# Kernel tuning notes

Hardware: AMD Instinct MI355X
Metric: run time of the kernel (lower is better)

Reference implementation:

```python
import jax, jax.numpy as jnp
import numpy as np

L, D, H, DK, FF, R, N, B = 8, 256, 8, 32, 1024, 37, 1024, 1
EPS = 1e-6


def setup_inputs() -> dict:
    key = jax.random.key(0)
    ks = jax.random.split(key, 16)
    def w(i, shape, s=0.05):
        return jax.random.normal(ks[i], shape, jnp.float32) * s
    return {
        "x": jax.random.normal(ks[0], (B, N, D), jnp.float32),
        "relations": jax.random.randint(ks[1], (N, N), 0, R),
        "Wq": w(2, (L, D, D)), "bq": jnp.zeros((L, D), jnp.float32),
        "Wk": w(3, (L, D, D)), "bk": jnp.zeros((L, D), jnp.float32),
        "Wv": w(4, (L, D, D)), "bv": jnp.zeros((L, D), jnp.float32),
        "Wo": w(5, (L, D, D)), "bo": jnp.zeros((L, D), jnp.float32),
        "rel_k_emb": w(6, (L, R, DK)), "rel_v_emb": w(7, (L, R, DK)),
        "W1": w(8, (L, D, FF)), "b1": jnp.zeros((L, FF), jnp.float32),
        "W2": w(9, (L, FF, D)), "b2": jnp.zeros((L, D), jnp.float32),
        "ln1_g": jnp.ones((L, D), jnp.float32), "ln1_b": jnp.zeros((L, D), jnp.float32),
        "ln2_g": jnp.ones((L, D), jnp.float32), "ln2_b": jnp.zeros((L, D), jnp.float32),
        "lnf_g": jnp.ones((D,), jnp.float32), "lnf_b": jnp.zeros((D,), jnp.float32),
    }


def _layernorm(h, g, b):
    # Annotated-Transformer LayerNorm: g*(x-mu)/(std+eps)+b with unbiased std
    mu = h.mean(-1, keepdims=True)
    sd = jnp.sqrt(h.var(-1, keepdims=True, ddof=1))
    return g * (h - mu) / (sd + EPS) + b


def reference(x, relations, Wq, bq, Wk, bk, Wv, bv, Wo, bo,
              rel_k_emb, rel_v_emb, W1, b1, W2, b2,
              ln1_g, ln1_b, ln2_g, ln2_b, lnf_g, lnf_b):
    Bb, n, d = x.shape
    scale = 1.0 / jnp.sqrt(jnp.float32(DK))
    for l in range(L):
        # --- relation-aware self-attention sublayer (pre-norm residual) ---
        xn = _layernorm(x, ln1_g[l], ln1_b[l])
        q = (xn @ Wq[l] + bq[l]).reshape(Bb, n, H, DK).transpose(0, 2, 1, 3)
        k = (xn @ Wk[l] + bk[l]).reshape(Bb, n, H, DK).transpose(0, 2, 1, 3)
        v = (xn @ Wv[l] + bv[l]).reshape(Bb, n, H, DK).transpose(0, 2, 1, 3)
        rk = rel_k_emb[l][relations]  # [n, n, DK] irregular gather
        rv = rel_v_emb[l][relations]  # [n, n, DK]
        scores = (jnp.einsum('bhid,bhjd->bhij', q, k)
                  + jnp.einsum('bhid,ijd->bhij', q, rk)) * scale
        p = jax.nn.softmax(scores, axis=-1)
        o = (jnp.einsum('bhij,bhjd->bhid', p, v)
             + jnp.einsum('bhij,ijd->bhid', p, rv))
        o = o.transpose(0, 2, 1, 3).reshape(Bb, n, d) @ Wo[l] + bo[l]
        x = x + o
        # --- position-wise FFN sublayer (pre-norm residual) ---
        xn = _layernorm(x, ln2_g[l], ln2_b[l])
        x = x + (jax.nn.relu(xn @ W1[l] + b1[l]) @ W2[l] + b2[l])
    return _layernorm(x, lnf_g, lnf_b)
```

## Files before the change

kernel.cpp:

```cpp
#include <hip/hip_runtime.h>
#include <stdint.h>

#define L_ 8
#define D_ 256
#define H_ 8
#define DK_ 32
#define FF_ 1024
#define R_ 37
#define N_ 1024
#define AIB 16

#define SCL (0.17677669529663689f * 1.4426950408889634f)

typedef float f4v __attribute__((ext_vector_type(4)));
typedef short b8v __attribute__((ext_vector_type(8)));
typedef uint  u2v __attribute__((ext_vector_type(2)));

__device__ __forceinline__ ushort f2b(float f){
  union { float f; uint32_t u; } x; x.f = f;
  return (ushort)((x.u + 0x7FFFu + ((x.u >> 16) & 1u)) >> 16);
}
__device__ __forceinline__ float b2f(ushort u){
  union { uint32_t u; float f; } x; x.u = ((uint32_t)u) << 16;
  return x.f;
}
__device__ __forceinline__ uint pk2b(float lo, float hi){
  return (((uint)f2b(hi)) << 16) | (uint)f2b(lo);
}
__device__ __forceinline__ float ex2(float x){ return __builtin_amdgcn_exp2f(x); }

__device__ __forceinline__ void lds_fadd(float* p, float v){
  asm volatile("ds_add_f32 %0, %1" :: "v"((uint)(uintptr_t)p), "v"(v) : "memory");
}

__global__ __launch_bounds__(256)
void wcast_kernel(const float* __restrict__ src, ushort* __restrict__ dst, int K, int Nc){
  __shared__ float t[32][33];
  int l = blockIdx.z;
  long base = (long)l * K * Nc;
  int n0 = blockIdx.x * 32, k0 = blockIdx.y * 32;
  int tx = threadIdx.x, ty = threadIdx.y;
  #pragma unroll
  for (int r = 0; r < 32; r += 8)
    t[ty + r][tx] = src[base + (long)(k0 + ty + r) * Nc + n0 + tx];
  __syncthreads();
  #pragma unroll
  for (int r = 0; r < 32; r += 8)
    dst[base + (long)(n0 + ty + r) * K + k0 + tx] = f2b(t[tx][ty + r]);
}

__global__ __launch_bounds__(256)
void rel8_kernel(const int* __restrict__ rel, uint* __restrict__ rel8){
  long idx = (long)blockIdx.x * 256 + threadIdx.x;
  int4 v = ((const int4*)rel)[idx];
  rel8[idx] = (uint)(v.x & 255) | ((uint)(v.y & 255) << 8)
            | ((uint)(v.z & 255) << 16) | ((uint)(v.w & 255) << 24);
}

template<int OUTB>
__global__ __launch_bounds__(64)
void ln_kernel(const float* __restrict__ x, const float* __restrict__ g, const float* __restrict__ b,
               ushort* __restrict__ ob, float* __restrict__ of){
  int row = blockIdx.x, lane = threadIdx.x;
  float4 v = ((const float4*)(x + (long)row * D_))[lane];
  float s = v.x + v.y + v.z + v.w;
  float s2 = v.x*v.x + v.y*v.y + v.z*v.z + v.w*v.w;
  #pragma unroll
  for (int o = 32; o; o >>= 1){ s += __shfl_xor(s, o); s2 += __shfl_xor(s2, o); }
  float mu = s * (1.f / D_);
  float var = (s2 - D_ * mu * mu) * (1.f / (D_ - 1));
  var = fmaxf(var, 0.f);
  float inv = 1.f / (sqrtf(var) + 1e-6f);
  float4 gv = ((const float4*)g)[lane];
  float4 bv = ((const float4*)b)[lane];
  float o0 = gv.x * (v.x - mu) * inv + bv.x;
  float o1 = gv.y * (v.y - mu) * inv + bv.y;
  float o2 = gv.z * (v.z - mu) * inv + bv.z;
  float o3 = gv.w * (v.w - mu) * inv + bv.w;
  if (OUTB){
    ushort4 u; u.x = f2b(o0); u.y = f2b(o1); u.z = f2b(o2); u.w = f2b(o3);
    ((ushort4*)ob)[(long)row * 64 + lane] = u;
  } else {
    float4 o; o.x = o0; o.y = o1; o.z = o2; o.w = o3;
    ((float4*)of)[(long)row * 64 + lane] = o;
  }
}

template<int QKV, int RELU, int RESID, int OUTF, int OUTB>
__global__ __launch_bounds__(256)
void gemm_kernel(const ushort* __restrict__ A,
                 const ushort* __restrict__ W0, const ushort* __restrict__ W1p, const ushort* __restrict__ W2p,
                 const float* __restrict__ B0, const float* __restrict__ B1p, const float* __restrict__ B2p,
                 float* __restrict__ resid, float* __restrict__ outF, ushort* __restrict__ outB,
                 ushort* __restrict__ outB2,
                 int M, int Nc, int K){
  __shared__ ushort Al[64 * 48];
  __shared__ ushort Bl[64 * 48];
  int tid = threadIdx.x;
  int lane = tid & 63, w = tid >> 6;
  int wm = w >> 1, wn = w & 1;
  int bn0 = blockIdx.x * 64, bm0 = blockIdx.y * 64;
  const ushort* WT; const float* bias; int wn0;
  if (QKV){
    int which = bn0 >> 8;
    WT = which == 0 ? W0 : (which == 1 ? W1p : W2p);
    bias = which == 0 ? B0 : (which == 1 ? B1p : B2p);
    wn0 = bn0 & 255;
  } else { WT = W0; bias = B0; wn0 = bn0; }

  int r4 = tid >> 2, c8 = (tid & 3) * 8;
  const ushort* ag = A + (long)(bm0 + r4) * K + c8;
  const ushort* bg = WT + (long)(wn0 + r4) * K + c8;

  f4v acc[2][2];
  #pragma unroll
  for (int i = 0; i < 2; ++i)
    #pragma unroll
    for (int j = 0; j < 2; ++j)
      acc[i][j] = (f4v){0.f, 0.f, 0.f, 0.f};

  int l16 = lane & 15, lg = lane >> 4;
  int arow0 = (wm * 32 + l16) * 48 + lg * 8;
  int brow0 = (wn * 32 + l16) * 48 + lg * 8;

  for (int k0 = 0; k0 < K; k0 += 32){
    b8v a8 = *(const b8v*)(ag + k0);
    b8v b8 = *(const b8v*)(bg + k0);
    __syncthreads();
    *(b8v*)&Al[r4 * 48 + c8] = a8;
    *(b8v*)&Bl[r4 * 48 + c8] = b8;
    __syncthreads();
    b8v a0 = *(const b8v*)&Al[arow0];
    b8v a1 = *(const b8v*)&Al[arow0 + 16 * 48];
    b8v b0 = *(const b8v*)&Bl[brow0];
    b8v b1 = *(const b8v*)&Bl[brow0 + 16 * 48];
    acc[0][0] = __builtin_amdgcn_mfma_f32_16x16x32_bf16(a0, b0, acc[0][0], 0, 0, 0);
    acc[0][1] = __builtin_amdgcn_mfma_f32_16x16x32_bf16(a0, b1, acc[0][1], 0, 0, 0);
    acc[1][0] = __builtin_amdgcn_mfma_f32_16x16x32_bf16(a1, b0, acc[1][0], 0, 0, 0);
    acc[1][1] = __builtin_amdgcn_mfma_f32_16x16x32_bf16(a1, b1, acc[1][1], 0, 0, 0);
  }
  #pragma unroll
  for (int fi = 0; fi < 2; ++fi)
    #pragma unroll
    for (int fj = 0; fj < 2; ++fj){
      int row0 = bm0 + wm * 32 + fi * 16 + lg * 4;
      int col = bn0 + wn * 32 + fj * 16 + l16;
      float vv[4];
      #pragma unroll
      for (int j = 0; j < 4; ++j) vv[j] = acc[fi][fj][j] + bias[QKV ? (col & 255) : col];
      if (QKV){
        int which = col >> 8, hh = (col >> 5) & 7, dk = col & 31;
        if (which == 2){
          ushort4 pk; pk.x = f2b(vv[0]); pk.y = f2b(vv[1]); pk.z = f2b(vv[2]); pk.w = f2b(vv[3]);
          *(ushort4*)(outB2 + (long)hh * 32768 + (long)dk * 1024 + row0) = pk;
        } else {
          #pragma unroll
          for (int j = 0; j < 4; ++j)
            outB[(long)which * 262144 + (long)hh * 32768 + (long)(row0 + j) * 32 + dk] = f2b(vv[j]);
        }
      } else {
        #pragma unroll
        for (int j = 0; j < 4; ++j){
          float v = vv[j];
          if (RELU) v = fmaxf(v, 0.f);
          long idx = (long)(row0 + j) * Nc + col;
          if (RESID) v += resid[idx];
          if (OUTF) outF[idx] = v;
          if (OUTB) outB[idx] = f2b(v);
        }
      }
    }
}

__global__ __launch_bounds__(512)
void attn_kernel(const ushort* __restrict__ qb, const ushort* __restrict__ kb,
                 const ushort* __restrict__ vbt, const float* __restrict__ rke,
                 const float* __restrict__ rve,
                 const unsigned char* __restrict__ rel8, ushort* __restrict__ ob){
  __shared__ float q_l[AIB * 32];
  __shared__ float qr_l[AIB * 40];
  __shared__ float prb[8 * AIB * 41];
  __shared__ uint  p_l[8 * AIB * 20];
  __shared__ float part_l[8 * AIB * 33];
  __shared__ float wf_l[8 * AIB];
  __shared__ float ls_l[8 * AIB];
  __shared__ float lrow_l[AIB];

  int tid = threadIdx.x, lane = tid & 63, w = tid >> 6;
  int l16 = lane & 15, g = lane >> 4;
  int ib0 = blockIdx.x * AIB, h = blockIdx.y;
  int ir = l16;

  if (tid < 128){
    int row = tid >> 3, d4 = (tid & 7) * 4;
    ushort4 u = *(const ushort4*)(qb + (long)((h << 10) + ib0 + row) * 32 + d4);
    q_l[row * 32 + d4 + 0] = b2f(u.x);
    q_l[row * 32 + d4 + 1] = b2f(u.y);
    q_l[row * 32 + d4 + 2] = b2f(u.z);
    q_l[row * 32 + d4 + 3] = b2f(u.w);
  }
  for (int idx = tid; idx < 8 * AIB * 41; idx += 512) prb[idx] = 0.f;
  __syncthreads();

  for (int slot = tid; slot < AIB * 40; slot += 512){
    int row = slot / 40, r = slot - row * 40;
    if (r < R_){
      const float* qh = &q_l[row * 32];
      const float* e = rke + r * 32;
      float acc = 0.f;
      #pragma unroll
      for (int d = 0; d < 32; ++d) acc += qh[d] * e[d];
      qr_l[slot] = acc * SCL;
    }
  }
  __syncthreads();

  b8v qf = *(const b8v*)(qb + (long)((h << 10) + ib0 + ir) * 32 + g * 8);

  f4v oacc0 = (f4v){0.f,0.f,0.f,0.f}, oacc1 = (f4v){0.f,0.f,0.f,0.f};
  float m = -3.0e38f;
  const float* qrr = &qr_l[ir * 40];
  float* prr = &prb[(w * AIB + ir) * 41];
  const unsigned char* relrow = rel8 + (long)(ib0 + ir) * N_ + w * 128;
  const ushort* kbh = kb + (long)(h << 10) * 32;
  const ushort* vth = vbt + (long)h * 32 * 1024;
  uint* pw = &p_l[(w * AIB + l16) * 20];

  uint raw[8];
  #pragma unroll
  for (int t = 0; t < 4; ++t){
    raw[t * 2]     = *(const uint*)(relrow + t * 32 + g * 4);
    raw[t * 2 + 1] = *(const uint*)(relrow + t * 32 + 16 + g * 4);
  }
  float qv[32];
  #pragma unroll
  for (int t = 0; t < 4; ++t)
    #pragma unroll
    for (int e = 0; e < 4; ++e){
      qv[t * 8 + e]     = qrr[(raw[t * 2]     >> (8 * e)) & 255];
      qv[t * 8 + 4 + e] = qrr[(raw[t * 2 + 1] >> (8 * e)) & 255];
    }

  int jb = w * 128;
  b8v kf0c = *(const b8v*)(kbh + (long)(jb + l16) * 32 + g * 8);
  b8v kf1c = *(const b8v*)(kbh + (long)(jb + 16 + l16) * 32 + g * 8);
  b8v vt0c = *(const b8v*)(vth + (long)l16 * 1024 + jb + g * 8);
  b8v vt1c = *(const b8v*)(vth + (long)(16 + l16) * 1024 + jb + g * 8);

  #pragma unroll
  for (int t = 0; t < 4; ++t){
    int j1 = jb + ((t + 1) & 3) * 32;
    b8v kf0n = *(const b8v*)(kbh + (long)(j1 + l16) * 32 + g * 8);
    b8v kf1n = *(const b8v*)(kbh + (long)(j1 + 16 + l16) * 32 + g * 8);
    b8v vt0n = *(const b8v*)(vth + (long)l16 * 1024 + j1 + g * 8);
    b8v vt1n = *(const b8v*)(vth + (long)(16 + l16) * 1024 + j1 + g * 8);

    f4v z = (f4v){0.f,0.f,0.f,0.f};
    f4v s0 = __builtin_amdgcn_mfma_f32_16x16x32_bf16(kf0c, qf, z, 0, 0, 0);
    f4v s1 = __builtin_amdgcn_mfma_f32_16x16x32_bf16(kf1c, qf, z, 0, 0, 0);

    float sv[8];
    #pragma unroll
    for (int e = 0; e < 4; ++e){
      sv[e]     = s0[e] * SCL + qv[t * 8 + e];
      sv[e + 4] = s1[e] * SCL + qv[t * 8 + 4 + e];
    }
    float lmax = sv[0];
    #pragma unroll
    for (int e = 1; e < 8; ++e) lmax = fmaxf(lmax, sv[e]);

    if (__any(lmax - m > 12.f)){
      float tmax = fmaxf(lmax, __shfl_xor(lmax, 16));
      tmax = fmaxf(tmax, __shfl_xor(tmax, 32));
      if (tmax > m){
        float f = ex2(m - tmax);
        oacc0 *= f; oacc1 *= f;
        #pragma unroll
        for (int b2 = 0; b2 < 10; ++b2){
          int bi = g * 10 + b2;
          if (bi < R_) prr[bi] *= f;
        }
        m = tmax;
      }
    }
    float p[8];
    #pragma unroll
    for (int e = 0; e < 8; ++e) p[e] = ex2(sv[e] - m);
    #pragma unroll
    for (int e = 0; e < 4; ++e){
      lds_fadd(&prr[(raw[t * 2]     >> (8 * e)) & 255], p[e]);
      lds_fadd(&prr[(raw[t * 2 + 1] >> (8 * e)) & 255], p[e + 4]);
    }

    uint pk0 = pk2b(p[0], p[1]), pk1 = pk2b(p[2], p[3]);
    uint pk2 = pk2b(p[4], p[5]), pk3 = pk2b(p[6], p[7]);
    *(u2v*)&pw[g * 2]     = (u2v){pk0, pk1};
    *(u2v*)&pw[8 + g * 2] = (u2v){pk2, pk3};
    b8v pf = *(const b8v*)&pw[g * 4];
    oacc0 = __builtin_amdgcn_mfma_f32_16x16x32_bf16(vt0c, pf, oacc0, 0, 0, 0);
    oacc1 = __builtin_amdgcn_mfma_f32_16x16x32_bf16(vt1c, pf, oacc1, 0, 0, 0);

    kf0c = kf0n; kf1c = kf1n; vt0c = vt0n; vt1c = vt1n;
  }

  {
    float* pp = &part_l[(w * AIB + ir) * 33];
    #pragma unroll
    for (int e = 0; e < 4; ++e){
      pp[g * 4 + e] = oacc0[e];
      pp[16 + g * 4 + e] = oacc1[e];
    }
    if (g == 0) pp[32] = m;
  }
  __syncthreads();

  for (int slot = tid; slot < 8 * AIB; slot += 512){
    const float* pb = &prb[slot * 41];
    float acc = 0.f;
    #pragma unroll
    for (int r = 0; r < R_; ++r) acc += pb[r];
    ls_l[slot] = acc;
  }
  __syncthreads();

  if (tid < AIB){
    int row = tid;
    float mstar = -3.0e38f;
    #pragma unroll
    for (int s = 0; s < 8; ++s) mstar = fmaxf(mstar, part_l[(s * AIB + row) * 33 + 32]);
    float lstar = 0.f;
    #pragma unroll
    for (int s = 0; s < 8; ++s){
      float wfv = ex2(part_l[(s * AIB + row) * 33 + 32] - mstar);
      wf_l[s * AIB + row] = wfv;
      lstar += ls_l[s * AIB + row] * wfv;
    }
    lrow_l[row] = lstar;
  }
  __syncthreads();

  for (int slot = tid; slot < AIB * 41; slot += 512){
    int row = slot / 41;
    float acc = 0.f;
    #pragma unroll
    for (int s = 0; s < 8; ++s) acc += prb[s * AIB * 41 + slot] * wf_l[s * AIB + row];
    prb[slot] = acc;
  }
  __syncthreads();

  {
    int row = tid >> 5, d = tid & 31;
    float o1 = 0.f;
    #pragma unroll
    for (int s = 0; s < 8; ++s) o1 += part_l[(s * AIB + row) * 33 + d] * wf_l[s * AIB + row];
    float o2 = 0.f;
    #pragma unroll
    for (int r = 0; r < R_; ++r) o2 += prb[row * 41 + r] * rve[r * 32 + d];
    float val = (o1 + o2) / lrow_l[row];
    ob[(long)(ib0 + row) * D_ + h * 32 + d] = f2b(val);
  }
}

extern "C" void kernel_launch(void* const* d_in, const int* in_sizes, int n_in,
                              void* d_out, int out_size, void* d_ws, size_t ws_size,
                              hipStream_t stream){
  const float* x    = (const float*)d_in[0];
  const int*   rel  = (const int*)d_in[1];
  const float* Wq   = (const float*)d_in[2];
  const float* bq   = (const float*)d_in[3];
  const float* Wk   = (const float*)d_in[4];
  const float* bk   = (const float*)d_in[5];
  const float* Wv   = (const float*)d_in[6];
  const float* bv   = (const float*)d_in[7];
  const float* Wo   = (const float*)d_in[8];
  const float* bo   = (const float*)d_in[9];
  const float* rke  = (const float*)d_in[10];
  const float* rve  = (const float*)d_in[11];
  const float* W1   = (const float*)d_in[12];
  const float* b1   = (const float*)d_in[13];
  const float* W2   = (const float*)d_in[14];
  const float* b2   = (const float*)d_in[15];
  const float* ln1g = (const float*)d_in[16];
  const float* ln1b = (const float*)d_in[17];
  const float* ln2g = (const float*)d_in[18];
  const float* ln2b = (const float*)d_in[19];
  const float* lnfg = (const float*)d_in[20];
  const float* lnfb = (const float*)d_in[21];

  char* wsb = (char*)d_ws;
  size_t off = 0;
  auto alloc = [&](size_t bytes){ void* p = wsb + off; off += (bytes + 255) & ~255ull; return p; };
  float*  xw   = (float*) alloc((size_t)N_ * D_ * 4);
  ushort* qkvb = (ushort*)alloc((size_t)3 * H_ * N_ * DK_ * 2);
  ushort* vbt  = (ushort*)alloc((size_t)H_ * DK_ * N_ * 2);
  ushort* xnb  = (ushort*)alloc((size_t)N_ * D_ * 2);
  ushort* obf  = (ushort*)alloc((size_t)N_ * D_ * 2);
  ushort* hidb = (ushort*)alloc((size_t)N_ * FF_ * 2);
  uint*   rel8 = (uint*)  alloc((size_t)N_ * N_);
  ushort* wqT  = (ushort*)alloc((size_t)L_ * D_ * D_ * 2);
  ushort* wkT  = (ushort*)alloc((size_t)L_ * D_ * D_ * 2);
  ushort* wvT  = (ushort*)alloc((size_t)L_ * D_ * D_ * 2);
  ushort* woT  = (ushort*)alloc((size_t)L_ * D_ * D_ * 2);
  ushort* w1T  = (ushort*)alloc((size_t)L_ * D_ * FF_ * 2);
  ushort* w2T  = (ushort*)alloc((size_t)L_ * D_ * FF_ * 2);
  (void)ws_size; (void)in_sizes; (void)n_in; (void)out_size;

  ushort* qb = qkvb;
  ushort* kb = qkvb + (size_t)H_ * N_ * DK_;

  dim3 tb(32, 8);
  wcast_kernel<<<dim3(D_/32,  D_/32,  L_), tb, 0, stream>>>(Wq, wqT, D_, D_);
  wcast_kernel<<<dim3(D_/32,  D_/32,  L_), tb, 0, stream>>>(Wk, wkT, D_, D_);
  wcast_kernel<<<dim3(D_/32,  D_/32,  L_), tb, 0, stream>>>(Wv, wvT, D_, D_);
  wcast_kernel<<<dim3(D_/32,  D_/32,  L_), tb, 0, stream>>>(Wo, woT, D_, D_);
  wcast_kernel<<<dim3(FF_/32, D_/32,  L_), tb, 0, stream>>>(W1, w1T, D_, FF_);
  wcast_kernel<<<dim3(D_/32,  FF_/32, L_), tb, 0, stream>>>(W2, w2T, FF_, D_);
  rel8_kernel<<<N_ * N_ / 1024, 256, 0, stream>>>(rel, rel8);

  hipMemcpyAsync(xw, x, (size_t)N_ * D_ * 4, hipMemcpyDeviceToDevice, stream);

  for (int l = 0; l < L_; ++l){
    ln_kernel<1><<<N_, 64, 0, stream>>>(xw, ln1g + l * D_, ln1b + l * D_, xnb, nullptr);
    gemm_kernel<1,0,0,0,1><<<dim3(768/64, N_/64), 256, 0, stream>>>(
        xnb, wqT + (size_t)l * D_ * D_, wkT + (size_t)l * D_ * D_, wvT + (size_t)l * D_ * D_,
        bq + l * D_, bk + l * D_, bv + l * D_,
        nullptr, nullptr, qkvb, vbt, N_, 768, D_);
    attn_kernel<<<dim3(N_/AIB, H_), 512, 0, stream>>>(
        qb, kb, vbt, rke + (size_t)l * R_ * DK_, rve + (size_t)l * R_ * DK_,
        (const unsigned char*)rel8, obf);
    gemm_kernel<0,0,1,1,0><<<dim3(D_/64, N_/64), 256, 0, stream>>>(
        obf, woT + (size_t)l * D_ * D_, nullptr, nullptr,
        bo + l * D_, nullptr, nullptr,
        xw, xw, nullptr, nullptr, N_, D_, D_);
    ln_kernel<1><<<N_, 64, 0, stream>>>(xw, ln2g + l * D_, ln2b + l * D_, xnb, nullptr);
    gemm_kernel<0,1,0,0,1><<<dim3(FF_/64, N_/64), 256, 0, stream>>>(
        xnb, w1T + (size_t)l * D_ * FF_, nullptr, nullptr,
        b1 + l * FF_, nullptr, nullptr,
        nullptr, nullptr, hidb, nullptr, N_, FF_, D_);
    gemm_kernel<0,0,1,1,0><<<dim3(D_/64, N_/64), 256, 0, stream>>>(
        hidb, w2T + (size_t)l * FF_ * D_, nullptr, nullptr,
        b2 + l * D_, nullptr, nullptr,
        xw, xw, nullptr, nullptr, N_, D_, FF_);
  }
  ln_kernel<0><<<N_, 64, 0, stream>>>(xw, lnfg, lnfb, nullptr, (float*)d_out);
}
```

Measured before the change: 787.4 us.

## Process two 16-row query tiles per attention block to reuse K/V fragments

The attention kernel now handles 32 query rows per block instead of 16. Each wave keeps two sets of Q fragments, running maxima, accumulators and relation-bucket sums, and reuses the same loaded K and V fragments across both tiles. This halves the number of blocks and the global K/V loads per query row. In exchange it raises register pressure (two qv[32] arrays, extra accumulators) and LDS usage, which can reduce occupancy, and the grid shrinks to 32x8 blocks.

```diff
diff --git a/kernel.cpp b/kernel.cpp
--- a/kernel.cpp
+++ b/kernel.cpp
@@ -8,7 +8,7 @@
 #define FF_ 1024
 #define R_ 37
 #define N_ 1024
-#define AIB 16
+#define AIB 32
 
 #define SCL (0.17677669529663689f * 1.4426950408889634f)
 
@@ -180,7 +180,7 @@
   __shared__ float q_l[AIB * 32];
   __shared__ float qr_l[AIB * 40];
   __shared__ float prb[8 * AIB * 41];
-  __shared__ uint  p_l[8 * AIB * 20];
+  __shared__ uint  p_l[8 * 16 * 40];
   __shared__ float part_l[8 * AIB * 33];
   __shared__ float wf_l[8 * AIB];
   __shared__ float ls_l[8 * AIB];
@@ -189,9 +189,8 @@
   int tid = threadIdx.x, lane = tid & 63, w = tid >> 6;
   int l16 = lane & 15, g = lane >> 4;
   int ib0 = blockIdx.x * AIB, h = blockIdx.y;
-  int ir = l16;
-
-  if (tid < 128){
+
+  if (tid < 256){
     int row = tid >> 3, d4 = (tid & 7) * 4;
     ushort4 u = *(const ushort4*)(qb + (long)((h << 10) + ib0 + row) * 32 + d4);
     q_l[row * 32 + d4 + 0] = b2f(u.x);
@@ -215,33 +214,43 @@
   }
   __syncthreads();
 
-  b8v qf = *(const b8v*)(qb + (long)((h << 10) + ib0 + ir) * 32 + g * 8);
-
-  f4v oacc0 = (f4v){0.f,0.f,0.f,0.f}, oacc1 = (f4v){0.f,0.f,0.f,0.f};
-  float m = -3.0e38f;
-  const float* qrr = &qr_l[ir * 40];
-  float* prr = &prb[(w * AIB + ir) * 41];
-  const unsigned char* relrow = rel8 + (long)(ib0 + ir) * N_ + w * 128;
   const ushort* kbh = kb + (long)(h << 10) * 32;
   const ushort* vth = vbt + (long)h * 32 * 1024;
-  uint* pw = &p_l[(w * AIB + l16) * 20];
-
-  uint raw[8];
+  int jb = w * 128;
+
+  b8v qf0 = *(const b8v*)(qb + (long)((h << 10) + ib0 + l16) * 32 + g * 8);
+  b8v qf1 = *(const b8v*)(qb + (long)((h << 10) + ib0 + 16 + l16) * 32 + g * 8);
+
+  f4v o00 = (f4v){0,0,0,0}, o01 = (f4v){0,0,0,0};
+  f4v o10 = (f4v){0,0,0,0}, o11 = (f4v){0,0,0,0};
+  float m0 = -3.0e38f, m1 = -3.0e38f;
+  const float* qrr0 = &qr_l[l16 * 40];
+  const float* qrr1 = &qr_l[(16 + l16) * 40];
+  float* prr0 = &prb[(w * AIB + l16) * 41];
+  float* prr1 = &prb[(w * AIB + 16 + l16) * 41];
+  uint* pw = &p_l[(w * 16 + l16) * 40];
+
+  const unsigned char* relrow0 = rel8 + (long)(ib0 + l16) * N_ + jb;
+  const unsigned char* relrow1 = rel8 + (long)(ib0 + 16 + l16) * N_ + jb;
+  uint raw0[8], raw1[8];
   #pragma unroll
   for (int t = 0; t < 4; ++t){
-    raw[t * 2]     = *(const uint*)(relrow + t * 32 + g * 4);
-    raw[t * 2 + 1] = *(const uint*)(relrow + t * 32 + 16 + g * 4);
-  }
-  float qv[32];
+    raw0[t * 2]     = *(const uint*)(relrow0 + t * 32 + g * 4);
+    raw0[t * 2 + 1] = *(const uint*)(relrow0 + t * 32 + 16 + g * 4);
+    raw1[t * 2]     = *(const uint*)(relrow1 + t * 32 + g * 4);
+    raw1[t * 2 + 1] = *(const uint*)(relrow1 + t * 32 + 16 + g * 4);
+  }
+  float qv0[32], qv1[32];
   #pragma unroll
   for (int t = 0; t < 4; ++t)
     #pragma unroll
     for (int e = 0; e < 4; ++e){
-      qv[t * 8 + e]     = qrr[(raw[t * 2]     >> (8 * e)) & 255];
-      qv[t * 8 + 4 + e] = qrr[(raw[t * 2 + 1] >> (8 * e)) & 255];
-    }
-
-  int jb = w * 128;
+      qv0[t * 8 + e]     = qrr0[(raw0[t * 2]     >> (8 * e)) & 255];
+      qv0[t * 8 + 4 + e] = qrr0[(raw0[t * 2 + 1] >> (8 * e)) & 255];
+      qv1[t * 8 + e]     = qrr1[(raw1[t * 2]     >> (8 * e)) & 255];
+      qv1[t * 8 + 4 + e] = qrr1[(raw1[t * 2 + 1] >> (8 * e)) & 255];
+    }
+
   b8v kf0c = *(const b8v*)(kbh + (long)(jb + l16) * 32 + g * 8);
   b8v kf1c = *(const b8v*)(kbh + (long)(jb + 16 + l16) * 32 + g * 8);
   b8v vt0c = *(const b8v*)(vth + (long)l16 * 1024 + jb + g * 8);
@@ -255,71 +264,95 @@
     b8v vt0n = *(const b8v*)(vth + (long)l16 * 1024 + j1 + g * 8);
     b8v vt1n = *(const b8v*)(vth + (long)(16 + l16) * 1024 + j1 + g * 8);
 
-    f4v z = (f4v){0.f,0.f,0.f,0.f};
-    f4v s0 = __builtin_amdgcn_mfma_f32_16x16x32_bf16(kf0c, qf, z, 0, 0, 0);
-    f4v s1 = __builtin_amdgcn_mfma_f32_16x16x32_bf16(kf1c, qf, z, 0, 0, 0);
-
-    float sv[8];
+    f4v z = (f4v){0,0,0,0};
+    f4v s0 = __builtin_amdgcn_mfma_f32_16x16x32_bf16(kf0c, qf0, z, 0, 0, 0);
+    f4v s1 = __builtin_amdgcn_mfma_f32_16x16x32_bf16(kf1c, qf0, z, 0, 0, 0);
+    f4v s2 = __builtin_amdgcn_mfma_f32_16x16x32_bf16(kf0c, qf1, z, 0, 0, 0);
+    f4v s3 = __builtin_amdgcn_mfma_f32_16x16x32_bf16(kf1c, qf1, z, 0, 0, 0);
+
+    float sv0[8], sv1[8];
     #pragma unroll
     for (int e = 0; e < 4; ++e){
-      sv[e]     = s0[e] * SCL + qv[t * 8 + e];
-      sv[e + 4] = s1[e] * SCL + qv[t * 8 + 4 + e];
-    }
-    float lmax = sv[0];
-    #pragma unroll
-    for (int e = 1; e < 8; ++e) lmax = fmaxf(lmax, sv[e]);
-
-    if (__any(lmax - m > 12.f)){
-      float tmax = fmaxf(lmax, __shfl_xor(lmax, 16));
-      tmax = fmaxf(tmax, __shfl_xor(tmax, 32));
-      if (tmax > m){
-        float f = ex2(m - tmax);
-        oacc0 *= f; oacc1 *= f;
+      sv0[e]     = s0[e] * SCL + qv0[t * 8 + e];
+      sv0[e + 4] = s1[e] * SCL + qv0[t * 8 + 4 + e];
+      sv1[e]     = s2[e] * SCL + qv1[t * 8 + e];
+      sv1[e + 4] = s3[e] * SCL + qv1[t * 8 + 4 + e];
+    }
+    float lm0 = sv0[0], lm1 = sv1[0];
+    #pragma unroll
+    for (int e = 1; e < 8; ++e){ lm0 = fmaxf(lm0, sv0[e]); lm1 = fmaxf(lm1, sv1[e]); }
+
+    if (__any((lm0 - m0 > 12.f) || (lm1 - m1 > 12.f))){
+      float tm0 = fmaxf(lm0, __shfl_xor(lm0, 16));
+      tm0 = fmaxf(tm0, __shfl_xor(tm0, 32));
+      float tm1 = fmaxf(lm1, __shfl_xor(lm1, 16));
+      tm1 = fmaxf(tm1, __shfl_xor(tm1, 32));
+      if (tm0 > m0){
+        float f = ex2(m0 - tm0);
+        o00 *= f; o01 *= f;
         #pragma unroll
         for (int b2 = 0; b2 < 10; ++b2){
           int bi = g * 10 + b2;
-          if (bi < R_) prr[bi] *= f;
+          if (bi < R_) prr0[bi] *= f;
         }
-        m = tmax;
+        m0 = tm0;
       }
-    }
-    float p[8];
-    #pragma unroll
-    for (int e = 0; e < 8; ++e) p[e] = ex2(sv[e] - m);
+      if (tm1 > m1){
+        float f = ex2(m1 - tm1);
+        o10 *= f; o11 *= f;
+        #pragma unroll
+        for (int b2 = 0; b2 < 10; ++b2){
+          int bi = g * 10 + b2;
+          if (bi < R_) prr1[bi] *= f;
+        }
+        m1 = tm1;
+      }
+    }
+    float p0[8], p1[8];
+    #pragma unroll
+    for (int e = 0; e < 8; ++e){ p0[e] = ex2(sv0[e] - m0); p1[e] = ex2(sv1[e] - m1); }
     #pragma unroll
     for (int e = 0; e < 4; ++e){
-      lds_fadd(&prr[(raw[t * 2]     >> (8 * e)) & 255], p[e]);
-      lds_fadd(&prr[(raw[t * 2 + 1] >> (8 * e)) & 255], p[e + 4]);
-    }
-
-    uint pk0 = pk2b(p[0], p[1]), pk1 = pk2b(p[2], p[3]);
-    uint pk2 = pk2b(p[4], p[5]), pk3 = pk2b(p[6], p[7]);
-    *(u2v*)&pw[g * 2]     = (u2v){pk0, pk1};
-    *(u2v*)&pw[8 + g * 2] = (u2v){pk2, pk3};
-    b8v pf = *(const b8v*)&pw[g * 4];
-    oacc0 = __builtin_amdgcn_mfma_f32_16x16x32_bf16(vt0c, pf, oacc0, 0, 0, 0);
-    oacc1 = __builtin_amdgcn_mfma_f32_16x16x32_bf16(vt1c, pf, oacc1, 0, 0, 0);
+      lds_fadd(&prr0[(raw0[t * 2]     >> (8 * e)) & 255], p0[e]);
+      lds_fadd(&prr0[(raw0[t * 2 + 1] >> (8 * e)) & 255], p0[e + 4]);
+      lds_fadd(&prr1[(raw1[t * 2]     >> (8 * e)) & 255], p1[e]);
+      lds_fadd(&prr1[(raw1[t * 2 + 1] >> (8 * e)) & 255], p1[e + 4]);
+    }
+
+    *(u2v*)&pw[g * 2]      = (u2v){pk2b(p0[0], p0[1]), pk2b(p0[2], p0[3])};
+    *(u2v*)&pw[8 + g * 2]  = (u2v){pk2b(p0[4], p0[5]), pk2b(p0[6], p0[7])};
+    *(u2v*)&pw[20 + g * 2] = (u2v){pk2b(p1[0], p1[1]), pk2b(p1[2], p1[3])};
+    *(u2v*)&pw[28 + g * 2] = (u2v){pk2b(p1[4], p1[5]), pk2b(p1[6], p1[7])};
+    b8v pf0 = *(const b8v*)&pw[g * 4];
+    b8v pf1 = *(const b8v*)&pw[20 + g * 4];
+    o00 = __builtin_amdgcn_mfma_f32_16x16x32_bf16(vt0c, pf0, o00, 0, 0, 0);
+    o01 = __builtin_amdgcn_mfma_f32_16x16x32_bf16(vt1c, pf0, o01, 0, 0, 0);
+    o10 = __builtin_amdgcn_mfma_f32_16x16x32_bf16(vt0c, pf1, o10, 0, 0, 0);
+    o11 = __builtin_amdgcn_mfma_f32_16x16x32_bf16(vt1c, pf1, o11, 0, 0, 0);
 
     kf0c = kf0n; kf1c = kf1n; vt0c = vt0n; vt1c = vt1n;
   }
 
   {
-    float* pp = &part_l[(w * AIB + ir) * 33];
+    float* pp0 = &part_l[(w * AIB + l16) * 33];
+    float* pp1 = &part_l[(w * AIB + 16 + l16) * 33];
     #pragma unroll
     for (int e = 0; e < 4; ++e){
-      pp[g * 4 + e] = oacc0[e];
-      pp[16 + g * 4 + e] = oacc1[e];
-    }
-    if (g == 0) pp[32] = m;
-  }
-  __syncthreads();
-
-  for (int slot = tid; slot < 8 * AIB; slot += 512){
-    const float* pb = &prb[slot * 41];
+      pp0[g * 4 + e] = o00[e];
+      pp0[16 + g * 4 + e] = o01[e];
+      pp1[g * 4 + e] = o10[e];
+      pp1[16 + g * 4 + e] = o11[e];
+    }
+    if (g == 0){ pp0[32] = m0; pp1[32] = m1; }
+  }
+  __syncthreads();
+
+  if (tid < 8 * AIB){
+    const float* pb = &prb[tid * 41];
     float acc = 0.f;
     #pragma unroll
     for (int r = 0; r < R_; ++r) acc += pb[r];
-    ls_l[slot] = acc;
+    ls_l[tid] = acc;
   }
   __syncthreads();
 
@@ -348,8 +381,8 @@
   }
   __syncthreads();
 
-  {
-    int row = tid >> 5, d = tid & 31;
+  for (int slot = tid; slot < AIB * 32; slot += 512){
+    int row = slot >> 5, d = slot & 31;
     float o1 = 0.f;
     #pragma unroll
     for (int s = 0; s < 8; ++s) o1 += part_l[(s * AIB + row) * 33 + d] * wf_l[s * AIB + row];
```

Measured after the change: 805.3 us. 2.3% more time.
